# Optimization experiments

Measured on AMD Instinct MI355X. Metric: run time of the kernel, lower is better.

The kernel has to match this reference:

```python
import jax, jax.numpy as jnp
import numpy as np

E, H, I, T = 8, 2048, 1024, 16384  # experts, hidden, moe_intermediate, total tokens


def setup_inputs() -> dict:
    key = jax.random.key(0)
    k1, k2, k3, k4 = jax.random.split(key, 4)
    hidden_states = jax.random.normal(k1, (T, H), dtype=jnp.float32)
    # ragged per-expert token counts, summing exactly to T (tokens pre-sorted by expert)
    group_sizes = jnp.array([1024, 3072, 2048, 4096, 512, 1536, 2560, 1536], dtype=jnp.int32)
    std = 0.01  # nn.initializers.normal() default stddev
    gate_w = jax.random.normal(k2, (E, H, I), dtype=jnp.float32) * std
    up_w = jax.random.normal(k3, (E, H, I), dtype=jnp.float32) * std
    down_w = jax.random.normal(k4, (E, I, H), dtype=jnp.float32) * std
    return {"hidden_states": hidden_states, "gate_w": gate_w, "up_w": up_w,
            "down_w": down_w, "group_sizes": group_sizes}


def reference(hidden_states, gate_w, up_w, down_w, group_sizes):
    # grouped GEMM: rows of hidden_states are contiguous per-expert blocks of
    # sizes group_sizes[e]; each block is multiplied by that expert's kernel.
    g = jax.lax.ragged_dot(hidden_states, gate_w, group_sizes)   # [T, I]
    u = jax.lax.ragged_dot(hidden_states, up_w, group_sizes)     # [T, I]
    h = jax.nn.silu(g) * u                                       # SwiGLU gating
    return jax.lax.ragged_dot(h, down_w, group_sizes)            # [T, H]
```

## Files before the change

### kernel.cpp

```cpp
#include <hip/hip_runtime.h>
#include <hip/hip_bf16.h>

#define E_ 8
#define H_ 2048
#define I_ 1024
#define T_ 16384
#define BK 64
#define BM 256
#define MT_ (T_ / BM + E_)
#define SLOT 32768

typedef __bf16 bf16x8 __attribute__((ext_vector_type(8)));
typedef float f32x4 __attribute__((ext_vector_type(4)));

__device__ __forceinline__ unsigned short f2bf(float f) {
  unsigned int x = __float_as_uint(f);
  x += 0x7FFFu + ((x >> 16) & 1u);
  return (unsigned short)(x >> 16);
}

__device__ __forceinline__ void gl_lds16(const void* g, void* s) {
  __builtin_amdgcn_global_load_lds(
      (const __attribute__((address_space(1))) void*)g,
      (__attribute__((address_space(3))) void*)s, 16, 0, 0);
}

#define VMCNT4 asm volatile("s_waitcnt vmcnt(4)" ::: "memory")
#define BARRIER                      \
  do {                               \
    __builtin_amdgcn_s_barrier();    \
    __builtin_amdgcn_sched_barrier(0); \
  } while (0)

#define MFMA16(ACC, AF, BF)                                                     \
  do {                                                                          \
    __builtin_amdgcn_s_setprio(1);                                              \
    _Pragma("unroll") for (int ks = 0; ks < 2; ks++)                            \
    _Pragma("unroll") for (int mi = 0; mi < 4; mi++)                            \
    _Pragma("unroll") for (int ni = 0; ni < 2; ni++)                            \
      ACC[mi][ni] = __builtin_amdgcn_mfma_f32_16x16x32_bf16(                    \
          AF[mi][ks], BF[ni][ks], ACC[mi][ni], 0, 0, 0);                        \
    __builtin_amdgcn_s_setprio(0);                                              \
  } while (0)

__device__ __forceinline__ bool find_tile(const int* gs, int tile, int& e,
                                          int& row0, int& rowEnd) {
  int base = 0, tb = 0;
  e = -1;
  for (int i = 0; i < E_; i++) {
    int g = gs[i];
    int nt = (g + BM - 1) >> 8;
    if (e < 0 && tile < tb + nt) {
      e = i;
      row0 = base + (tile - tb) * BM;
      rowEnd = base + g;
    }
    tb += nt;
    base += g;
  }
  return e >= 0;
}


__global__ void cvt_hs(const float* __restrict__ in, ushort* __restrict__ out) {
  size_t i = ((size_t)blockIdx.x * 256 + threadIdx.x) * 8;
  float4 a = *(const float4*)(in + i);
  float4 b = *(const float4*)(in + i + 4);
  union { ushort u[8]; uint4 v; } p;
  p.u[0] = f2bf(a.x); p.u[1] = f2bf(a.y); p.u[2] = f2bf(a.z); p.u[3] = f2bf(a.w);
  p.u[4] = f2bf(b.x); p.u[5] = f2bf(b.y); p.u[6] = f2bf(b.z); p.u[7] = f2bf(b.w);
  *(uint4*)(out + i) = p.v;
}

__global__ void cvt_tr(const float* __restrict__ in, ushort* __restrict__ out,
                       int K, int N) {
  __shared__ ushort tile[64][65];
  int n0 = blockIdx.x * 64, k0 = blockIdx.y * 64;
  const float* src = in + (size_t)blockIdx.z * K * N;
  ushort* dst = out + (size_t)blockIdx.z * K * N;
  int t = threadIdx.x;
  int rb = t >> 4, c4 = (t & 15) * 4;
#pragma unroll
  for (int i = 0; i < 4; i++) {
    int r = rb + i * 16;
    float4 v = *(const float4*)(src + (size_t)(k0 + r) * N + n0 + c4);
    tile[r][c4 + 0] = f2bf(v.x);
    tile[r][c4 + 1] = f2bf(v.y);
    tile[r][c4 + 2] = f2bf(v.z);
    tile[r][c4 + 3] = f2bf(v.w);
  }
  __syncthreads();
#pragma unroll
  for (int i = 0; i < 2; i++) {
    int c = t + i * 256;
    int n = c >> 3, kc = c & 7;
    union { ushort u[8]; uint4 v; } p;
#pragma unroll
    for (int j = 0; j < 8; j++) p.u[j] = tile[kc * 8 + j][n];
    *(uint4*)(dst + (size_t)(n0 + n) * K + k0 + kc * 8) = p.v;
  }
}

__global__ __launch_bounds__(512, 2) void gemm_gateup(
    const ushort* __restrict__ A, const ushort* __restrict__ BgT,
    const ushort* __restrict__ BuT, const int* __restrict__ gs,
    ushort* __restrict__ Hb) {
  extern __shared__ __align__(16) ushort ls[];

  int e, row0, rowEnd;
  if (!find_tile(gs, blockIdx.x, e, row0, rowEnd)) return;
  const int n0 = blockIdx.y * 128;

  const int t = threadIdx.x;
  const int lane = t & 63;
  const int w = t >> 6;
  const int wm = w & 1, wn = w >> 1;
  const int ldW = w * 512;

  int oAlo[2], oAhi[2], oB[2];
#pragma unroll
  for (int l = 0; l < 2; l++) {
    int c = l * 512 + t;
    int r = c >> 3, kc = (c & 7) ^ (r & 7);
    int a0 = row0 + r;       if (a0 > T_ - 1) a0 = T_ - 1;
    int a1 = row0 + 128 + r; if (a1 > T_ - 1) a1 = T_ - 1;
    oAlo[l] = a0 * H_ + kc * 8;
    oAhi[l] = a1 * H_ + kc * 8;
    oB[l] = (e * I_ + n0 + r) * H_ + kc * 8;
  }

  const int l15 = lane & 15, l7 = lane & 7, lk = lane >> 4;
  const int s0 = (lk ^ l7) * 8, s1 = ((lk + 4) ^ l7) * 8;
  const int arow = (wm * 64 + l15) * 64;
  const int brow = (wn * 32 + l15) * 64;

  f32x4 accG0[4][2], accG1[4][2], accU0[4][2], accU1[4][2];
#pragma unroll
  for (int mi = 0; mi < 4; mi++)
#pragma unroll
    for (int ni = 0; ni < 2; ni++) {
      accG0[mi][ni] = (f32x4){0.f, 0.f, 0.f, 0.f};
      accG1[mi][ni] = (f32x4){0.f, 0.f, 0.f, 0.f};
      accU0[mi][ni] = (f32x4){0.f, 0.f, 0.f, 0.f};
      accU1[mi][ni] = (f32x4){0.f, 0.f, 0.f, 0.f};
    }

  gl_lds16(A + oAlo[0], ls + 0 + ldW);
  gl_lds16(A + oAlo[1], ls + 4096 + ldW);
  gl_lds16(BgT + oB[0], ls + 16384 + ldW);
  gl_lds16(BgT + oB[1], ls + 16384 + 4096 + ldW);
  gl_lds16(BuT + oB[0], ls + 24576 + ldW);
  gl_lds16(BuT + oB[1], ls + 24576 + 4096 + ldW);
  gl_lds16(A + oAhi[0], ls + 8192 + ldW);
  gl_lds16(A + oAhi[1], ls + 8192 + 4096 + ldW);

#pragma unroll 2
  for (int tt = 0; tt < H_ / BK; tt++) {
    const int p = tt & 1, q = p ^ 1;
    const ushort* sa = ls + p * SLOT;
    ushort* sq = ls + q * SLOT;
    const int kn = (tt + 1 < H_ / BK ? tt + 1 : tt) * BK;
    bf16x8 af[4][2], gf[2][2], uf[2][2];

    VMCNT4; BARRIER;
    gl_lds16(A + oAlo[0] + kn, sq + 0 + ldW);
    gl_lds16(A + oAlo[1] + kn, sq + 4096 + ldW);
#pragma unroll
    for (int mi = 0; mi < 4; mi++) {
      af[mi][0] = *(const bf16x8*)(sa + arow + mi * 1024 + s0);
      af[mi][1] = *(const bf16x8*)(sa + arow + mi * 1024 + s1);
    }
#pragma unroll
    for (int ni = 0; ni < 2; ni++) {
      gf[ni][0] = *(const bf16x8*)(sa + 16384 + brow + ni * 1024 + s0);
      gf[ni][1] = *(const bf16x8*)(sa + 16384 + brow + ni * 1024 + s1);
    }
    MFMA16(accG0, af, gf);

    VMCNT4; BARRIER;
    gl_lds16(BgT + oB[0] + kn, sq + 16384 + ldW);
    gl_lds16(BgT + oB[1] + kn, sq + 16384 + 4096 + ldW);
#pragma unroll
    for (int ni = 0; ni < 2; ni++) {
      uf[ni][0] = *(const bf16x8*)(sa + 24576 + brow + ni * 1024 + s0);
      uf[ni][1] = *(const bf16x8*)(sa + 24576 + brow + ni * 1024 + s1);
    }
    MFMA16(accU0, af, uf);

    VMCNT4; BARRIER;
    gl_lds16(BuT + oB[0] + kn, sq + 24576 + ldW);
    gl_lds16(BuT + oB[1] + kn, sq + 24576 + 4096 + ldW);
#pragma unroll
    for (int mi = 0; mi < 4; mi++) {
      af[mi][0] = *(const bf16x8*)(sa + 8192 + arow + mi * 1024 + s0);
      af[mi][1] = *(const bf16x8*)(sa + 8192 + arow + mi * 1024 + s1);
    }
    MFMA16(accG1, af, gf);

    BARRIER;
    gl_lds16(A + oAhi[0] + kn, sq + 8192 + ldW);
    gl_lds16(A + oAhi[1] + kn, sq + 8192 + 4096 + ldW);
    MFMA16(accU1, af, uf);
  }

  const int cr = row0 + wm * 64 + (lk << 2);
  const int cc = n0 + wn * 32 + l15;
#pragma unroll
  for (int mh = 0; mh < 2; mh++)
#pragma unroll
    for (int mi = 0; mi < 4; mi++)
#pragma unroll
      for (int ni = 0; ni < 2; ni++)
#pragma unroll
        for (int r = 0; r < 4; r++) {
          int row = cr + mh * 128 + mi * 16 + r;
          if (row < rowEnd) {
            float g = mh ? accG1[mi][ni][r] : accG0[mi][ni][r];
            float u = mh ? accU1[mi][ni][r] : accU0[mi][ni][r];
            float h = (g / (1.0f + __expf(-g))) * u;
            Hb[(size_t)row * I_ + cc + ni * 16] = f2bf(h);
          }
        }
}

__global__ __launch_bounds__(512, 2) void gemm_down(
    const ushort* __restrict__ A, const ushort* __restrict__ BdT,
    const int* __restrict__ gs, float* __restrict__ Out) {
  extern __shared__ __align__(16) ushort ls[];

  int e, row0, rowEnd;
  if (!find_tile(gs, blockIdx.x, e, row0, rowEnd)) return;
  const int n0 = blockIdx.y * 256;

  const int t = threadIdx.x;
  const int lane = t & 63;
  const int w = t >> 6;
  const int wm = w & 1, wn = w >> 1;
  const int ldW = w * 512;

  int oAlo[2], oAhi[2], oBlo[2], oBhi[2];
#pragma unroll
  for (int l = 0; l < 2; l++) {
    int c = l * 512 + t;
    int r = c >> 3, kc = (c & 7) ^ (r & 7);
    int a0 = row0 + r;       if (a0 > T_ - 1) a0 = T_ - 1;
    int a1 = row0 + 128 + r; if (a1 > T_ - 1) a1 = T_ - 1;
    oAlo[l] = a0 * I_ + kc * 8;
    oAhi[l] = a1 * I_ + kc * 8;
    oBlo[l] = (e * H_ + n0 + r) * I_ + kc * 8;
    oBhi[l] = (e * H_ + n0 + 128 + r) * I_ + kc * 8;
  }

  const int l15 = lane & 15, l7 = lane & 7, lk = lane >> 4;
  const int s0 = (lk ^ l7) * 8, s1 = ((lk + 4) ^ l7) * 8;
  const int arow = (wm * 64 + l15) * 64;
  const int brow = (wn * 32 + l15) * 64;

  f32x4 acc00[4][2], acc01[4][2], acc11[4][2], acc10[4][2];
#pragma unroll
  for (int mi = 0; mi < 4; mi++)
#pragma unroll
    for (int ni = 0; ni < 2; ni++) {
      acc00[mi][ni] = (f32x4){0.f, 0.f, 0.f, 0.f};
      acc01[mi][ni] = (f32x4){0.f, 0.f, 0.f, 0.f};
      acc11[mi][ni] = (f32x4){0.f, 0.f, 0.f, 0.f};
      acc10[mi][ni] = (f32x4){0.f, 0.f, 0.f, 0.f};
    }

  gl_lds16(A + oAlo[0], ls + 0 + ldW);
  gl_lds16(A + oAlo[1], ls + 4096 + ldW);
  gl_lds16(BdT + oBlo[0], ls + 16384 + ldW);
  gl_lds16(BdT + oBlo[1], ls + 16384 + 4096 + ldW);
  gl_lds16(BdT + oBhi[0], ls + 24576 + ldW);
  gl_lds16(BdT + oBhi[1], ls + 24576 + 4096 + ldW);
  gl_lds16(A + oAhi[0], ls + 8192 + ldW);
  gl_lds16(A + oAhi[1], ls + 8192 + 4096 + ldW);

#pragma unroll 2
  for (int tt = 0; tt < I_ / BK; tt++) {
    const int p = tt & 1, q = p ^ 1;
    const ushort* sa = ls + p * SLOT;
    ushort* sq = ls + q * SLOT;
    const int kn = (tt + 1 < I_ / BK ? tt + 1 : tt) * BK;
    bf16x8 af[4][2], bf0[2][2], bf1[2][2];

    VMCNT4; BARRIER;
    gl_lds16(A + oAlo[0] + kn, sq + 0 + ldW);
    gl_lds16(A + oAlo[1] + kn, sq + 4096 + ldW);
#pragma unroll
    for (int mi = 0; mi < 4; mi++) {
      af[mi][0] = *(const bf16x8*)(sa + arow + mi * 1024 + s0);
      af[mi][1] = *(const bf16x8*)(sa + arow + mi * 1024 + s1);
    }
#pragma unroll
    for (int ni = 0; ni < 2; ni++) {
      bf0[ni][0] = *(const bf16x8*)(sa + 16384 + brow + ni * 1024 + s0);
      bf0[ni][1] = *(const bf16x8*)(sa + 16384 + brow + ni * 1024 + s1);
    }
    MFMA16(acc00, af, bf0);

    VMCNT4; BARRIER;
    gl_lds16(BdT + oBlo[0] + kn, sq + 16384 + ldW);
    gl_lds16(BdT + oBlo[1] + kn, sq + 16384 + 4096 + ldW);
#pragma unroll
    for (int ni = 0; ni < 2; ni++) {
      bf1[ni][0] = *(const bf16x8*)(sa + 16384 + 8192 + brow + ni * 1024 + s0);
      bf1[ni][1] = *(const bf16x8*)(sa + 16384 + 8192 + brow + ni * 1024 + s1);
    }
    MFMA16(acc01, af, bf1);

    VMCNT4; BARRIER;
    gl_lds16(BdT + oBhi[0] + kn, sq + 24576 + ldW);
    gl_lds16(BdT + oBhi[1] + kn, sq + 24576 + 4096 + ldW);
#pragma unroll
    for (int mi = 0; mi < 4; mi++) {
      af[mi][0] = *(const bf16x8*)(sa + 8192 + arow + mi * 1024 + s0);
      af[mi][1] = *(const bf16x8*)(sa + 8192 + arow + mi * 1024 + s1);
    }
    MFMA16(acc11, af, bf1);

    BARRIER;
    gl_lds16(A + oAhi[0] + kn, sq + 8192 + ldW);
    gl_lds16(A + oAhi[1] + kn, sq + 8192 + 4096 + ldW);
    MFMA16(acc10, af, bf0);
  }

  const int cr = row0 + wm * 64 + (lk << 2);
  const int cc = n0 + wn * 32 + l15;
#pragma unroll
  for (int mh = 0; mh < 2; mh++)
#pragma unroll
    for (int mi = 0; mi < 4; mi++)
#pragma unroll
      for (int nh = 0; nh < 2; nh++)
#pragma unroll
        for (int ni = 0; ni < 2; ni++)
#pragma unroll
          for (int r = 0; r < 4; r++) {
            int row = cr + mh * 128 + mi * 16 + r;
            if (row < rowEnd) {
              float v = mh ? (nh ? acc11[mi][ni][r] : acc10[mi][ni][r])
                           : (nh ? acc01[mi][ni][r] : acc00[mi][ni][r]);
              Out[(size_t)row * H_ + cc + nh * 128 + ni * 16] = v;
            }
          }
}

extern "C" void kernel_launch(void* const* d_in, const int* in_sizes, int n_in,
                              void* d_out, int out_size, void* d_ws, size_t ws_size,
                              hipStream_t stream) {
  const float* hs = (const float*)d_in[0];
  const float* gw = (const float*)d_in[1];
  const float* uw = (const float*)d_in[2];
  const float* dw = (const float*)d_in[3];
  const int* gs = (const int*)d_in[4];
  float* out = (float*)d_out;

  ushort* hsb = (ushort*)d_ws;
  ushort* wgT = hsb + (size_t)T_ * H_;
  ushort* wuT = wgT + (size_t)E_ * H_ * I_;
  ushort* wdT = wuT + (size_t)E_ * H_ * I_;
  ushort* hb  = wdT + (size_t)E_ * H_ * I_;

  (void)hipFuncSetAttribute(reinterpret_cast<const void*>(gemm_gateup),
                            hipFuncAttributeMaxDynamicSharedMemorySize, 131072);
  (void)hipFuncSetAttribute(reinterpret_cast<const void*>(gemm_down),
                            hipFuncAttributeMaxDynamicSharedMemorySize, 131072);

  cvt_hs<<<((size_t)T_ * H_) / (256 * 8), 256, 0, stream>>>(hs, hsb);
  cvt_tr<<<dim3(I_ / 64, H_ / 64, E_), 256, 0, stream>>>(gw, wgT, H_, I_);
  cvt_tr<<<dim3(I_ / 64, H_ / 64, E_), 256, 0, stream>>>(uw, wuT, H_, I_);
  cvt_tr<<<dim3(H_ / 64, I_ / 64, E_), 256, 0, stream>>>(dw, wdT, I_, H_);

  gemm_gateup<<<dim3(MT_, I_ / 128), 512, 131072, stream>>>(hsb, wgT, wuT, gs, hb);
  gemm_down<<<dim3(MT_, H_ / 256), 512, 131072, stream>>>(hb, wdT, gs, out);
}
```

Before: 546.0 us.

## Prefetch next-stage LDS fragments into registers across loop iterations

Both grouped-GEMM kernels now keep separate register fragments for the low and high A halves and both B tiles. Each LDS fragment load is issued one MFMA block ahead, including a prologue load and a cross-iteration prefetch of the next buffer's A-low and B-low fragments. Wait counts are relaxed from vmcnt(4) to vmcnt(2) at the matching points. The aim is to hide LDS read latency behind MFMA work, at the cost of higher register pressure and tighter ordering between the barriers and the async global-to-LDS copies.

Result: slower. 756.7 us (+38.6%).

```diff
diff --git a/kernel.cpp b/kernel.cpp
--- a/kernel.cpp
+++ b/kernel.cpp
@@ -25,10 +25,11 @@
       (__attribute__((address_space(3))) void*)s, 16, 0, 0);
 }
 
+#define VMCNT2 asm volatile("s_waitcnt vmcnt(2)" ::: "memory")
 #define VMCNT4 asm volatile("s_waitcnt vmcnt(4)" ::: "memory")
-#define BARRIER                      \
-  do {                               \
-    __builtin_amdgcn_s_barrier();    \
+#define BARRIER                        \
+  do {                                 \
+    __builtin_amdgcn_s_barrier();      \
     __builtin_amdgcn_sched_barrier(0); \
   } while (0)
 
@@ -145,6 +146,8 @@
       accU1[mi][ni] = (f32x4){0.f, 0.f, 0.f, 0.f};
     }
 
+  bf16x8 afL[4][2], afH[4][2], gf[2][2], uf[2][2];
+
   gl_lds16(A + oAlo[0], ls + 0 + ldW);
   gl_lds16(A + oAlo[1], ls + 4096 + ldW);
   gl_lds16(BgT + oB[0], ls + 16384 + ldW);
@@ -153,6 +156,17 @@
   gl_lds16(BuT + oB[1], ls + 24576 + 4096 + ldW);
   gl_lds16(A + oAhi[0], ls + 8192 + ldW);
   gl_lds16(A + oAhi[1], ls + 8192 + 4096 + ldW);
+  VMCNT4; BARRIER;
+#pragma unroll
+  for (int mi = 0; mi < 4; mi++) {
+    afL[mi][0] = *(const bf16x8*)(ls + arow + mi * 1024 + s0);
+    afL[mi][1] = *(const bf16x8*)(ls + arow + mi * 1024 + s1);
+  }
+#pragma unroll
+  for (int ni = 0; ni < 2; ni++) {
+    gf[ni][0] = *(const bf16x8*)(ls + 16384 + brow + ni * 1024 + s0);
+    gf[ni][1] = *(const bf16x8*)(ls + 16384 + brow + ni * 1024 + s1);
+  }
 
 #pragma unroll 2
   for (int tt = 0; tt < H_ / BK; tt++) {
@@ -160,47 +174,46 @@
     const ushort* sa = ls + p * SLOT;
     ushort* sq = ls + q * SLOT;
     const int kn = (tt + 1 < H_ / BK ? tt + 1 : tt) * BK;
-    bf16x8 af[4][2], gf[2][2], uf[2][2];
-
-    VMCNT4; BARRIER;
+
+    VMCNT2; BARRIER;
     gl_lds16(A + oAlo[0] + kn, sq + 0 + ldW);
     gl_lds16(A + oAlo[1] + kn, sq + 4096 + ldW);
 #pragma unroll
-    for (int mi = 0; mi < 4; mi++) {
-      af[mi][0] = *(const bf16x8*)(sa + arow + mi * 1024 + s0);
-      af[mi][1] = *(const bf16x8*)(sa + arow + mi * 1024 + s1);
-    }
-#pragma unroll
-    for (int ni = 0; ni < 2; ni++) {
-      gf[ni][0] = *(const bf16x8*)(sa + 16384 + brow + ni * 1024 + s0);
-      gf[ni][1] = *(const bf16x8*)(sa + 16384 + brow + ni * 1024 + s1);
-    }
-    MFMA16(accG0, af, gf);
-
-    VMCNT4; BARRIER;
+    for (int ni = 0; ni < 2; ni++) {
+      uf[ni][0] = *(const bf16x8*)(sa + 24576 + brow + ni * 1024 + s0);
+      uf[ni][1] = *(const bf16x8*)(sa + 24576 + brow + ni * 1024 + s1);
+    }
+    MFMA16(accG0, afL, gf);
+
+    VMCNT2; BARRIER;
     gl_lds16(BgT + oB[0] + kn, sq + 16384 + ldW);
     gl_lds16(BgT + oB[1] + kn, sq + 16384 + 4096 + ldW);
 #pragma unroll
-    for (int ni = 0; ni < 2; ni++) {
-      uf[ni][0] = *(const bf16x8*)(sa + 24576 + brow + ni * 1024 + s0);
-      uf[ni][1] = *(const bf16x8*)(sa + 24576 + brow + ni * 1024 + s1);
-    }
-    MFMA16(accU0, af, uf);
-
-    VMCNT4; BARRIER;
+    for (int mi = 0; mi < 4; mi++) {
+      afH[mi][0] = *(const bf16x8*)(sa + 8192 + arow + mi * 1024 + s0);
+      afH[mi][1] = *(const bf16x8*)(sa + 8192 + arow + mi * 1024 + s1);
+    }
+    MFMA16(accU0, afL, uf);
+
+    BARRIER;
     gl_lds16(BuT + oB[0] + kn, sq + 24576 + ldW);
     gl_lds16(BuT + oB[1] + kn, sq + 24576 + 4096 + ldW);
-#pragma unroll
-    for (int mi = 0; mi < 4; mi++) {
-      af[mi][0] = *(const bf16x8*)(sa + 8192 + arow + mi * 1024 + s0);
-      af[mi][1] = *(const bf16x8*)(sa + 8192 + arow + mi * 1024 + s1);
-    }
-    MFMA16(accG1, af, gf);
-
-    BARRIER;
+    MFMA16(accG1, afH, gf);
+
+    VMCNT2; BARRIER;
     gl_lds16(A + oAhi[0] + kn, sq + 8192 + ldW);
     gl_lds16(A + oAhi[1] + kn, sq + 8192 + 4096 + ldW);
-    MFMA16(accU1, af, uf);
+#pragma unroll
+    for (int mi = 0; mi < 4; mi++) {
+      afL[mi][0] = *(const bf16x8*)(sq + arow + mi * 1024 + s0);
+      afL[mi][1] = *(const bf16x8*)(sq + arow + mi * 1024 + s1);
+    }
+#pragma unroll
+    for (int ni = 0; ni < 2; ni++) {
+      gf[ni][0] = *(const bf16x8*)(sq + 16384 + brow + ni * 1024 + s0);
+      gf[ni][1] = *(const bf16x8*)(sq + 16384 + brow + ni * 1024 + s1);
+    }
+    MFMA16(accU1, afH, uf);
   }
 
   const int cr = row0 + wm * 64 + (lk << 2);
@@ -256,16 +269,18 @@
   const int arow = (wm * 64 + l15) * 64;
   const int brow = (wn * 32 + l15) * 64;
 
-  f32x4 acc00[4][2], acc01[4][2], acc11[4][2], acc10[4][2];
+  f32x4 acc00[4][2], acc01[4][2], acc10[4][2], acc11[4][2];
 #pragma unroll
   for (int mi = 0; mi < 4; mi++)
 #pragma unroll
     for (int ni = 0; ni < 2; ni++) {
       acc00[mi][ni] = (f32x4){0.f, 0.f, 0.f, 0.f};
       acc01[mi][ni] = (f32x4){0.f, 0.f, 0.f, 0.f};
+      acc10[mi][ni] = (f32x4){0.f, 0.f, 0.f, 0.f};
       acc11[mi][ni] = (f32x4){0.f, 0.f, 0.f, 0.f};
-      acc10[mi][ni] = (f32x4){0.f, 0.f, 0.f, 0.f};
-    }
+    }
+
+  bf16x8 afL[4][2], afH[4][2], bfL[2][2], bfH[2][2];
 
   gl_lds16(A + oAlo[0], ls + 0 + ldW);
   gl_lds16(A + oAlo[1], ls + 4096 + ldW);
@@ -275,6 +290,17 @@
   gl_lds16(BdT + oBhi[1], ls + 24576 + 4096 + ldW);
   gl_lds16(A + oAhi[0], ls + 8192 + ldW);
   gl_lds16(A + oAhi[1], ls + 8192 + 4096 + ldW);
+  VMCNT4; BARRIER;
+#pragma unroll
+  for (int mi = 0; mi < 4; mi++) {
+    afL[mi][0] = *(const bf16x8*)(ls + arow + mi * 1024 + s0);
+    afL[mi][1] = *(const bf16x8*)(ls + arow + mi * 1024 + s1);
+  }
+#pragma unroll
+  for (int ni = 0; ni < 2; ni++) {
+    bfL[ni][0] = *(const bf16x8*)(ls + 16384 + brow + ni * 1024 + s0);
+    bfL[ni][1] = *(const bf16x8*)(ls + 16384 + brow + ni * 1024 + s1);
+  }
 
 #pragma unroll 2
   for (int tt = 0; tt < I_ / BK; tt++) {
@@ -282,47 +308,46 @@
     const ushort* sa = ls + p * SLOT;
     ushort* sq = ls + q * SLOT;
     const int kn = (tt + 1 < I_ / BK ? tt + 1 : tt) * BK;
-    bf16x8 af[4][2], bf0[2][2], bf1[2][2];
-
-    VMCNT4; BARRIER;
+
+    VMCNT2; BARRIER;
     gl_lds16(A + oAlo[0] + kn, sq + 0 + ldW);
     gl_lds16(A + oAlo[1] + kn, sq + 4096 + ldW);
 #pragma unroll
-    for (int mi = 0; mi < 4; mi++) {
-      af[mi][0] = *(const bf16x8*)(sa + arow + mi * 1024 + s0);
-      af[mi][1] = *(const bf16x8*)(sa + arow + mi * 1024 + s1);
-    }
-#pragma unroll
-    for (int ni = 0; ni < 2; ni++) {
-      bf0[ni][0] = *(const bf16x8*)(sa + 16384 + brow + ni * 1024 + s0);
-      bf0[ni][1] = *(const bf16x8*)(sa + 16384 + brow + ni * 1024 + s1);
-    }
-    MFMA16(acc00, af, bf0);
-
-    VMCNT4; BARRIER;
+    for (int ni = 0; ni < 2; ni++) {
+      bfH[ni][0] = *(const bf16x8*)(sa + 24576 + brow + ni * 1024 + s0);
+      bfH[ni][1] = *(const bf16x8*)(sa + 24576 + brow + ni * 1024 + s1);
+    }
+    MFMA16(acc00, afL, bfL);
+
+    VMCNT2; BARRIER;
     gl_lds16(BdT + oBlo[0] + kn, sq + 16384 + ldW);
     gl_lds16(BdT + oBlo[1] + kn, sq + 16384 + 4096 + ldW);
 #pragma unroll
-    for (int ni = 0; ni < 2; ni++) {
-      bf1[ni][0] = *(const bf16x8*)(sa + 16384 + 8192 + brow + ni * 1024 + s0);
-      bf1[ni][1] = *(const bf16x8*)(sa + 16384 + 8192 + brow + ni * 1024 + s1);
-    }
-    MFMA16(acc01, af, bf1);
-
-    VMCNT4; BARRIER;
+    for (int mi = 0; mi < 4; mi++) {
+      afH[mi][0] = *(const bf16x8*)(sa + 8192 + arow + mi * 1024 + s0);
+      afH[mi][1] = *(const bf16x8*)(sa + 8192 + arow + mi * 1024 + s1);
+    }
+    MFMA16(acc01, afL, bfH);
+
+    BARRIER;
     gl_lds16(BdT + oBhi[0] + kn, sq + 24576 + ldW);
     gl_lds16(BdT + oBhi[1] + kn, sq + 24576 + 4096 + ldW);
-#pragma unroll
-    for (int mi = 0; mi < 4; mi++) {
-      af[mi][0] = *(const bf16x8*)(sa + 8192 + arow + mi * 1024 + s0);
-      af[mi][1] = *(const bf16x8*)(sa + 8192 + arow + mi * 1024 + s1);
-    }
-    MFMA16(acc11, af, bf1);
-
-    BARRIER;
+    MFMA16(acc10, afH, bfL);
+
+    VMCNT2; BARRIER;
     gl_lds16(A + oAhi[0] + kn, sq + 8192 + ldW);
     gl_lds16(A + oAhi[1] + kn, sq + 8192 + 4096 + ldW);
-    MFMA16(acc10, af, bf0);
+#pragma unroll
+    for (int mi = 0; mi < 4; mi++) {
+      afL[mi][0] = *(const bf16x8*)(sq + arow + mi * 1024 + s0);
+      afL[mi][1] = *(const bf16x8*)(sq + arow + mi * 1024 + s1);
+    }
+#pragma unroll
+    for (int ni = 0; ni < 2; ni++) {
+      bfL[ni][0] = *(const bf16x8*)(sq + 16384 + brow + ni * 1024 + s0);
+      bfL[ni][1] = *(const bf16x8*)(sq + 16384 + brow + ni * 1024 + s1);
+    }
+    MFMA16(acc11, afH, bfH);
   }
 
   const int cr = row0 + wm * 64 + (lk << 2);
```
